# Optimization experiments

Measured on AMD Instinct MI355X. Metric: run time of the kernel, lower is better.

The kernel has to match this reference:

```python
import jax, jax.numpy as jnp
import numpy as np

B, S, M, E, H = 2, 2048, 2048, 1024, 16
D = E // H
LN_EPS = 1e-5


def setup_inputs() -> dict:
    key = jax.random.key(0)
    ks = jax.random.split(key, 14)
    w = lambda k: jax.random.normal(k, (E, E), dtype=jnp.float32) * 0.02
    return {
        "query": jax.random.normal(ks[0], (B, S, E), dtype=jnp.float32),
        "keys": jax.random.normal(ks[1], (B, M, E), dtype=jnp.float32),
        "values": jax.random.normal(ks[2], (B, M, E), dtype=jnp.float32),
        "Wq": w(ks[3]), "bq": jnp.zeros((E,), jnp.float32),
        "Wk": w(ks[4]), "bk": jnp.zeros((E,), jnp.float32),
        "Wv": w(ks[5]), "bv": jnp.zeros((E,), jnp.float32),
        "Wo": w(ks[6]), "bo": jnp.zeros((E,), jnp.float32),
        "gamma": jnp.ones((E,), jnp.float32),
        "beta": jnp.zeros((E,), jnp.float32),
    }


def reference(query, keys, values, Wq, bq, Wk, bk, Wv, bv, Wo, bo, gamma, beta):
    b, s, e = query.shape
    m = keys.shape[1]
    # projections (torch Linear: x @ W.T + b), split heads -> [b, H, len, D]
    Q = (jnp.einsum('bse,fe->bsf', query, Wq) + bq).reshape(b, s, H, D).transpose(0, 2, 1, 3)
    K = (jnp.einsum('bme,fe->bmf', keys, Wk) + bk).reshape(b, m, H, D).transpose(0, 2, 1, 3)
    V = (jnp.einsum('bme,fe->bmf', values, Wv) + bv).reshape(b, m, H, D).transpose(0, 2, 1, 3)
    scores = jnp.einsum('bhsd,bhmd->bhsm', Q, K) / np.sqrt(D).astype(np.float32)
    attn = jax.nn.softmax(scores, axis=-1)  # [b,H,s,m]; dropout is eval no-op
    attended = jnp.einsum('bhsm,bhmd->bhsd', attn, V)
    attended = attended.transpose(0, 2, 1, 3).reshape(b, s, e)
    y = jnp.einsum('bse,fe->bsf', attended, Wo) + bo + query
    mu = jnp.mean(y, axis=-1, keepdims=True)
    var = jnp.mean(jnp.square(y - mu), axis=-1, keepdims=True)
    out = (y - mu) * jax.lax.rsqrt(var + LN_EPS) * gamma + beta
    avg_attention = attn.mean(axis=1)  # [b,s,m]
    return out, avg_attention
```

## Files before the change

kernel.cpp:

```cpp
#include <hip/hip_runtime.h>
#include <hip/hip_bf16.h>

typedef unsigned short u16;
typedef unsigned int   u32;
typedef __attribute__((ext_vector_type(2)))  float fx2;
typedef __attribute__((ext_vector_type(4)))  float fx4;
typedef __attribute__((ext_vector_type(16))) float f32x16;
typedef __attribute__((ext_vector_type(4)))  u16   usx4;
typedef __attribute__((ext_vector_type(8)))  u16   usx8;
typedef __attribute__((ext_vector_type(8)))  __bf16 bf16x8;
typedef __attribute__((ext_vector_type(2)))  int   i32x2;
typedef __attribute__((ext_vector_type(2)))  u32   u32x2;
typedef __attribute__((ext_vector_type(4)))  u32   u32x4;

#define DEVI static __device__ __forceinline__

constexpr int Bb = 2, Ss = 2048, Mm = 2048, Ee = 1024, Hh = 16, Dd = 64;
#define QSCALE 0.18033688011112042f

DEVI u16 f2bf(float f) {
  u32 u = __builtin_bit_cast(u32, f);
  u32 r = (u + 0x7fffu + ((u >> 16) & 1u)) >> 16;
  return (u16)r;
}
DEVI bf16x8 as_bf(usx8 v) { return __builtin_bit_cast(bf16x8, v); }

DEVI void gld16(const u16* g, u16* l) {
  __builtin_amdgcn_global_load_lds((const __attribute__((address_space(1))) void*)g,
                                   (__attribute__((address_space(3))) void*)l, 16, 0, 0);
}

#if __has_builtin(__builtin_amdgcn_exp2f)
DEVI float xexp2(float x) { return __builtin_amdgcn_exp2f(x); }
#else
DEVI float xexp2(float x) { return exp2f(x); }
#endif

DEVI u32 cvtpk(float lo, float hi) {
  u32 r;
  asm("v_cvt_pk_bf16_f32 %0, %1, %2" : "=v"(r) : "v"(lo), "v"(hi));
  return r;
}
DEVI bf16x8 pa_from(u32 w0, u32 w1, u32 w2, u32 w3) {
  union { u32 u[4]; usx8 v; } t;
  t.u[0] = w0; t.u[1] = w1; t.u[2] = w2; t.u[3] = w3;
  return as_bf(t.v);
}

__global__ __launch_bounds__(256)
void cast_all(const float* __restrict__ q, const float* __restrict__ k,
              const float* __restrict__ v,
              const float* __restrict__ wq, const float* __restrict__ wk,
              const float* __restrict__ wv, const float* __restrict__ wo,
              u16* __restrict__ qc, u16* __restrict__ kc, u16* __restrict__ vc,
              u16* __restrict__ wqc, u16* __restrict__ wkc,
              u16* __restrict__ wvc, u16* __restrict__ woc)
{
  const int y = blockIdx.y;
  const float* s; u16* d; size_t n;
  const size_t NI = (size_t)Bb * Ss * Ee;
  const size_t NW = (size_t)Ee * Ee;
  switch (y) {
    case 0: s = q;  d = qc;  n = NI; break;
    case 1: s = k;  d = kc;  n = NI; break;
    case 2: s = v;  d = vc;  n = NI; break;
    case 3: s = wq; d = wqc; n = NW; break;
    case 4: s = wk; d = wkc; n = NW; break;
    case 5: s = wv; d = wvc; n = NW; break;
    default: s = wo; d = woc; n = NW; break;
  }
  const size_t stride = (size_t)gridDim.x * 256 * 8;
  for (size_t i = ((size_t)blockIdx.x * 256 + threadIdx.x) * 8; i < n; i += stride) {
    fx4 a = *(const fx4*)(s + i);
    fx4 b = *(const fx4*)(s + i + 4);
    u32x4 o;
    o[0] = cvtpk(a[0], a[1]); o[1] = cvtpk(a[2], a[3]);
    o[2] = cvtpk(b[0], b[1]); o[3] = cvtpk(b[2], b[3]);
    *(u32x4*)(d + i) = o;
  }
}

__global__ __launch_bounds__(256, 2)
void gemm_qkv(const u16* __restrict__ qc, const u16* __restrict__ kc,
              const u16* __restrict__ vc,
              const u16* __restrict__ wqc, const u16* __restrict__ wkc,
              const u16* __restrict__ wvc,
              const float* __restrict__ bq, const float* __restrict__ bk,
              const float* __restrict__ bv,
              u16* __restrict__ Qbf, u16* __restrict__ Kbf, u16* __restrict__ Vt)
{
  __shared__ u16 As[2][128][64];
  __shared__ u16 Bs[2][128][64];
  const int tid = threadIdx.x;
  const int w = tid >> 6, l = tid & 63, g = l >> 4, ln = l & 15;
  const int wr = w >> 1, wc = w & 1;

  const int lid = blockIdx.x;
  const int wg = (lid & 7) * 96 + (lid >> 3);
  const int z = wg >> 8;
  const int rem = wg & 255;
  const int row0 = (rem >> 3) * 128;
  const int col0 = (rem & 7) * 128;

  const u16* A = (z == 0) ? qc : (z == 1) ? kc : vc;
  const u16* W = (z == 0) ? wqc : (z == 1) ? wkc : wvc;
  const float* bias = (z == 0) ? bq : (z == 1) ? bk : bv;

  const int colu = (((l & 7) ^ (l >> 3)) << 3);
  auto stage = [&](int buf, int kt) {
#pragma unroll
    for (int j = 0; j < 4; j++) {
      const int c = j * 4 + w;
      const int row = c * 8 + (l >> 3);
      gld16(A + (size_t)(row0 + row) * 1024 + kt * 64 + colu,
            &As[buf][0][0] + c * 512 + l * 8);
      gld16(W + (size_t)(col0 + row) * 1024 + kt * 64 + colu,
            &Bs[buf][0][0] + c * 512 + l * 8);
    }
  };

  fx4 acc[4][4];
#pragma unroll
  for (int i = 0; i < 4; i++)
#pragma unroll
    for (int j = 0; j < 4; j++) acc[i][j] = fx4{0.f, 0.f, 0.f, 0.f};

  stage(0, 0);
  __syncthreads();

  const int swA = (ln & 7) << 3;
  const int NK = 1024 / 64;
  for (int kt = 0; kt < NK; kt++) {
    const int buf = kt & 1;
    if (kt + 1 < NK) stage(buf ^ 1, kt + 1);
#pragma unroll
    for (int ks = 0; ks < 2; ks++) {
      bf16x8 af[4], bfr[4];
      const int cb = (ks * 32 + g * 8) ^ swA;
#pragma unroll
      for (int mi = 0; mi < 4; mi++)
        af[mi] = as_bf(*(const usx8*)&As[buf][wr * 64 + mi * 16 + ln][cb]);
#pragma unroll
      for (int nj = 0; nj < 4; nj++)
        bfr[nj] = as_bf(*(const usx8*)&Bs[buf][wc * 64 + nj * 16 + ln][cb]);
      __builtin_amdgcn_s_setprio(1);
#pragma unroll
      for (int mi = 0; mi < 4; mi++)
#pragma unroll
        for (int nj = 0; nj < 4; nj++)
          acc[mi][nj] = __builtin_amdgcn_mfma_f32_16x16x32_bf16(af[mi], bfr[nj], acc[mi][nj], 0, 0, 0);
      __builtin_amdgcn_s_setprio(0);
    }
    __syncthreads();
  }

#pragma unroll
  for (int mi = 0; mi < 4; mi++) {
#pragma unroll
    for (int nj = 0; nj < 4; nj++) {
      const int j = col0 + wc * 64 + nj * 16 + ln;
      const float bj = bias[j];
      if (z == 2) {
        const int i0 = row0 + wr * 64 + mi * 16 + g * 4;
        const int b2 = i0 >> 11, m2 = i0 & 2047;
        const int h2 = j >> 6,  d2 = j & 63;
        u32x2 pk;
        pk[0] = cvtpk(acc[mi][nj][0] + bj, acc[mi][nj][1] + bj);
        pk[1] = cvtpk(acc[mi][nj][2] + bj, acc[mi][nj][3] + bj);
        *(u32x2*)&Vt[(((size_t)b2 * Hh + h2) * 64 + d2) * (size_t)Mm + m2] = pk;
      } else {
        u16* outp = (z == 0) ? Qbf : Kbf;
        const float sc = (z == 0) ? QSCALE : 1.0f;
#pragma unroll
        for (int r = 0; r < 4; r++) {
          const int i = row0 + wr * 64 + mi * 16 + g * 4 + r;
          outp[(size_t)i * 1024 + j] = f2bf((acc[mi][nj][r] + bj) * sc);
        }
      }
    }
  }
}

__global__ __launch_bounds__(256, 2)
void gemm_out(const u16* __restrict__ Ab, const u16* __restrict__ W,
              const float* __restrict__ bias, const float* __restrict__ resid,
              float* __restrict__ outf)
{
  __shared__ u16 As[2][128][64];
  __shared__ u16 Bs[2][128][64];
  const int tid = threadIdx.x;
  const int w = tid >> 6, l = tid & 63, g = l >> 4, ln = l & 15;
  const int wr = w >> 1, wc = w & 1;

  const int lid = blockIdx.x;
  const int wg = (lid & 7) * 32 + (lid >> 3);
  const int row0 = (wg >> 3) * 128;
  const int col0 = (wg & 7) * 128;

  const int colu = (((l & 7) ^ (l >> 3)) << 3);
  auto stage = [&](int buf, int kt) {
#pragma unroll
    for (int j = 0; j < 4; j++) {
      const int c = j * 4 + w;
      const int row = c * 8 + (l >> 3);
      gld16(Ab + (size_t)(row0 + row) * 1024 + kt * 64 + colu,
            &As[buf][0][0] + c * 512 + l * 8);
      gld16(W + (size_t)(col0 + row) * 1024 + kt * 64 + colu,
            &Bs[buf][0][0] + c * 512 + l * 8);
    }
  };

  fx4 acc[4][4];
#pragma unroll
  for (int i = 0; i < 4; i++)
#pragma unroll
    for (int j = 0; j < 4; j++) acc[i][j] = fx4{0.f, 0.f, 0.f, 0.f};

  stage(0, 0);
  __syncthreads();

  const int swA = (ln & 7) << 3;
  const int NK = 1024 / 64;
  for (int kt = 0; kt < NK; kt++) {
    const int buf = kt & 1;
    if (kt + 1 < NK) stage(buf ^ 1, kt + 1);
#pragma unroll
    for (int ks = 0; ks < 2; ks++) {
      bf16x8 af[4], bfr[4];
      const int cb = (ks * 32 + g * 8) ^ swA;
#pragma unroll
      for (int mi = 0; mi < 4; mi++)
        af[mi] = as_bf(*(const usx8*)&As[buf][wr * 64 + mi * 16 + ln][cb]);
#pragma unroll
      for (int nj = 0; nj < 4; nj++)
        bfr[nj] = as_bf(*(const usx8*)&Bs[buf][wc * 64 + nj * 16 + ln][cb]);
      __builtin_amdgcn_s_setprio(1);
#pragma unroll
      for (int mi = 0; mi < 4; mi++)
#pragma unroll
        for (int nj = 0; nj < 4; nj++)
          acc[mi][nj] = __builtin_amdgcn_mfma_f32_16x16x32_bf16(af[mi], bfr[nj], acc[mi][nj], 0, 0, 0);
      __builtin_amdgcn_s_setprio(0);
    }
    __syncthreads();
  }

#pragma unroll
  for (int mi = 0; mi < 4; mi++) {
#pragma unroll
    for (int nj = 0; nj < 4; nj++) {
      const int j = col0 + wc * 64 + nj * 16 + ln;
      const float bj = bias[j];
#pragma unroll
      for (int r = 0; r < 4; r++) {
        const int i = row0 + wr * 64 + mi * 16 + g * 4 + r;
        outf[(size_t)i * 1024 + j] = acc[mi][nj][r] + bj + resid[(size_t)i * 1024 + j];
      }
    }
  }
}

__global__ __launch_bounds__(256, 2)
void flash_fwd(const u16* __restrict__ Qb, const u16* __restrict__ Kb,
               const u16* __restrict__ Vt, u16* __restrict__ attended,
               float* __restrict__ stats)
{
  __shared__ u16 Ks[2][128][64];
  __shared__ u16 Vs[2][64][128];
  const int tid = threadIdx.x;
  const int w = tid >> 6, l = tid & 63;
  const int ln32 = l & 31, hi = l >> 5;
  const int st = blockIdx.x, h = blockIdx.y, b = blockIdx.z;
  const int s0 = st * 128 + w * 32;

  const u16* Kbase = Kb + (size_t)b * Mm * 1024 + h * 64;
  const u16* Vbase = Vt + ((size_t)(b * Hh + h) * 64) * (size_t)Mm;

  const int colu_k = (((l & 7) ^ (l >> 3)) << 3);
  auto stage = [&](int buf, int mt) {
    const int mb = mt * 128;
#pragma unroll
    for (int j = 0; j < 4; j++) {
      const int c = j * 4 + w;
      const int krow = c * 8 + (l >> 3);
      gld16(Kbase + (size_t)(mb + krow) * 1024 + colu_k,
            &Ks[buf][0][0] + c * 512 + l * 8);
      const int vrow = c * 4 + (l >> 4);
      const int colv = (((l & 15) ^ (vrow & 15)) << 3);
      gld16(Vbase + (size_t)vrow * (size_t)Mm + mb + colv,
            &Vs[buf][0][0] + c * 512 + l * 8);
    }
  };

  bf16x8 qa[4];
#pragma unroll
  for (int dstep = 0; dstep < 4; dstep++)
    qa[dstep] = as_bf(*(const usx8*)(Qb + (size_t)(b * Ss + s0 + ln32) * Ee
                                     + h * 64 + dstep * 16 + hi * 8));

  f32x16 acc[2];
#pragma unroll
  for (int i = 0; i < 16; i++) { acc[0][i] = 0.f; acc[1][i] = 0.f; }
  float lsum = 0.f;

  stage(0, 0);
  __syncthreads();

  const int NT = Mm / 128;
  for (int mt = 0; mt < NT; mt++) {
    const int buf = mt & 1;
    if (mt + 1 < NT) stage(buf ^ 1, mt + 1);

    f32x16 sc[4];
#pragma unroll
    for (int mtile = 0; mtile < 4; mtile++) {
      const int row = mtile * 32 + ln32;
      const int sw = (row & 7) << 3;
      f32x16 c;
#pragma unroll
      for (int i = 0; i < 16; i++) c[i] = 0.f;
#pragma unroll
      for (int dstep = 0; dstep < 4; dstep++) {
        bf16x8 kf = as_bf(*(const usx8*)&Ks[buf][row][(dstep * 16 + hi * 8) ^ sw]);
        c = __builtin_amdgcn_mfma_f32_32x32x16_bf16(kf, qa[dstep], c, 0, 0, 0);
      }
      sc[mtile] = c;
    }

#pragma unroll
    for (int mtile = 0; mtile < 4; mtile++) {
      float p[16];
#pragma unroll
      for (int r = 0; r < 16; r++) p[r] = xexp2(sc[mtile][r]);
      float t0 = (p[0] + p[1]) + (p[2] + p[3]);
      float t1 = (p[4] + p[5]) + (p[6] + p[7]);
      float t2 = (p[8] + p[9]) + (p[10] + p[11]);
      float t3 = (p[12] + p[13]) + (p[14] + p[15]);
      lsum += (t0 + t1) + (t2 + t3);

      u32 cp[8];
#pragma unroll
      for (int i = 0; i < 8; i++) cp[i] = cvtpk(p[2 * i], p[2 * i + 1]);
      i32x2 sA = __builtin_amdgcn_permlane32_swap((int)cp[0], (int)cp[2], false, false);
      i32x2 sB = __builtin_amdgcn_permlane32_swap((int)cp[1], (int)cp[3], false, false);
      bf16x8 pa0 = pa_from((u32)sA.x, (u32)sB.x, (u32)sA.y, (u32)sB.y);
      i32x2 sC = __builtin_amdgcn_permlane32_swap((int)cp[4], (int)cp[6], false, false);
      i32x2 sD = __builtin_amdgcn_permlane32_swap((int)cp[5], (int)cp[7], false, false);
      bf16x8 pa1 = pa_from((u32)sC.x, (u32)sD.x, (u32)sC.y, (u32)sD.y);

#pragma unroll
      for (int dtile = 0; dtile < 2; dtile++) {
        const int vrow = dtile * 32 + ln32;
        const int vsw = (vrow & 15) << 3;
        bf16x8 vb0 = as_bf(*(const usx8*)&Vs[buf][vrow][(mtile * 32 + hi * 8) ^ vsw]);
        bf16x8 vb1 = as_bf(*(const usx8*)&Vs[buf][vrow][(mtile * 32 + 16 + hi * 8) ^ vsw]);
        acc[dtile] = __builtin_amdgcn_mfma_f32_32x32x16_bf16(pa0, vb0, acc[dtile], 0, 0, 0);
        acc[dtile] = __builtin_amdgcn_mfma_f32_32x32x16_bf16(pa1, vb1, acc[dtile], 0, 0, 0);
      }
    }
    __syncthreads();
  }

  lsum += __shfl_xor(lsum, 32);
  const float inv = 1.0f / lsum;
  if (l < 32)
    stats[(size_t)(b * Hh + h) * Ss + s0 + l] = inv;
#pragma unroll
  for (int r = 0; r < 16; r++) {
    const int srow = (r & 3) + 8 * (r >> 2) + 4 * hi;
    const float invr = __shfl(inv, srow);
    const int s_abs = s0 + srow;
#pragma unroll
    for (int dtile = 0; dtile < 2; dtile++)
      attended[(size_t)(b * Ss + s_abs) * Ee + h * 64 + dtile * 32 + ln32] =
          f2bf(acc[dtile][r] * invr);
  }
}

__global__ __launch_bounds__(256)
void avg_attn(const u16* __restrict__ Qb, const u16* __restrict__ Kb,
              const float* __restrict__ stats, float* __restrict__ avg_out)
{
  __shared__ u16 Ks[2][64][64];
  const int tid = threadIdx.x;
  const int w = tid >> 6, l = tid & 63;
  const int ln32 = l & 31, hi = l >> 5;
  const int mtile0 = blockIdx.x, stile = blockIdx.y, b = blockIdx.z;
  const int m0 = mtile0 * 64;
  const int s0 = stile * 128 + w * 32;
  const int s_lane = s0 + ln32;

  const u16* Kbase = Kb + (size_t)(b * Mm + m0) * 1024;
  const u16* Qrow  = Qb + (size_t)(b * Ss + s_lane) * Ee;
  const float* strow = stats + (size_t)b * Hh * Ss + s_lane;

  const int colu = (((l & 7) ^ (l >> 3)) << 3);
  auto stage = [&](int buf, int h) {
#pragma unroll
    for (int j = 0; j < 2; j++) {
      const int c = j * 4 + w;
      const int row = c * 8 + (l >> 3);
      u16* kdst = &Ks[buf][0][0] + c * 512 + l * 8;
      gld16(Kbase + (size_t)row * 1024 + h * 64 + colu, kdst);
    }
  };

  f32x16 acc[2];
#pragma unroll
  for (int i = 0; i < 16; i++) { acc[0][i] = 0.f; acc[1][i] = 0.f; }

  stage(0, 0);
  __syncthreads();

  for (int h = 0; h < Hh; h++) {
    const int buf = h & 1;
    if (h + 1 < Hh) stage(buf ^ 1, h + 1);

    bf16x8 qa[4];
#pragma unroll
    for (int dstep = 0; dstep < 4; dstep++)
      qa[dstep] = as_bf(*(const usx8*)(Qrow + h * 64 + dstep * 16 + hi * 8));
    const float invh = strow[(size_t)h * Ss];

#pragma unroll
    for (int mtile = 0; mtile < 2; mtile++) {
      const int row = mtile * 32 + ln32;
      const int sw = (row & 7) << 3;
      f32x16 c;
#pragma unroll
      for (int i = 0; i < 16; i++) c[i] = 0.f;
      __builtin_amdgcn_s_setprio(1);
#pragma unroll
      for (int dstep = 0; dstep < 4; dstep++) {
        bf16x8 kf = as_bf(*(const usx8*)&Ks[buf][row][(dstep * 16 + hi * 8) ^ sw]);
        c = __builtin_amdgcn_mfma_f32_32x32x16_bf16(kf, qa[dstep], c, 0, 0, 0);
      }
      __builtin_amdgcn_s_setprio(0);
#pragma unroll
      for (int r = 0; r < 16; r++)
        acc[mtile][r] += xexp2(c[r]) * invh;
    }
    __syncthreads();
  }

  float* orow = avg_out + ((size_t)(b * Ss + s_lane)) * Mm + m0;
#pragma unroll
  for (int mtile = 0; mtile < 2; mtile++)
#pragma unroll
    for (int rq = 0; rq < 4; rq++) {
      fx4 o;
#pragma unroll
      for (int j = 0; j < 4; j++) o[j] = acc[mtile][rq * 4 + j] * (1.0f / 16.0f);
      *(fx4*)(orow + mtile * 32 + rq * 8 + 4 * hi) = o;
    }
}

__global__ __launch_bounds__(256)
void ln_kernel(const float* __restrict__ y, const float* __restrict__ gamma,
               const float* __restrict__ beta, float* __restrict__ out)
{
  const int row = blockIdx.x, tid = threadIdx.x;
  const int w = tid >> 6, l = tid & 63;
  fx4 v = *(const fx4*)(y + (size_t)row * 1024 + tid * 4);
  float s = v[0] + v[1] + v[2] + v[3];
  float s2 = v[0] * v[0] + v[1] * v[1] + v[2] * v[2] + v[3] * v[3];
#pragma unroll
  for (int off = 32; off >= 1; off >>= 1) {
    s += __shfl_xor(s, off);
    s2 += __shfl_xor(s2, off);
  }
  __shared__ float rs[4], rq[4];
  if (l == 0) { rs[w] = s; rq[w] = s2; }
  __syncthreads();
  s = (rs[0] + rs[1]) + (rs[2] + rs[3]);
  s2 = (rq[0] + rq[1]) + (rq[2] + rq[3]);
  const float mu = s * (1.0f / 1024.0f);
  const float var = s2 * (1.0f / 1024.0f) - mu * mu;
  const float rstd = rsqrtf(var + 1e-5f);
  fx4 gm = *(const fx4*)(gamma + tid * 4);
  fx4 bt = *(const fx4*)(beta + tid * 4);
  fx4 o;
#pragma unroll
  for (int j = 0; j < 4; j++) o[j] = (v[j] - mu) * rstd * gm[j] + bt[j];
  *(fx4*)(out + (size_t)row * 1024 + tid * 4) = o;
}

extern "C" void kernel_launch(void* const* d_in, const int* in_sizes, int n_in,
                              void* d_out, int out_size, void* d_ws, size_t ws_size,
                              hipStream_t stream)
{
  const float* query = (const float*)d_in[0];
  const float* keys  = (const float*)d_in[1];
  const float* values = (const float*)d_in[2];
  const float* Wq = (const float*)d_in[3];  const float* bq = (const float*)d_in[4];
  const float* Wk = (const float*)d_in[5];  const float* bk = (const float*)d_in[6];
  const float* Wv = (const float*)d_in[7];  const float* bv = (const float*)d_in[8];
  const float* Wo = (const float*)d_in[9];  const float* bo = (const float*)d_in[10];
  const float* gamma = (const float*)d_in[11];
  const float* beta  = (const float*)d_in[12];

  float* out = (float*)d_out;
  float* avg_out = out + (size_t)Bb * Ss * Ee;

  const size_t MB = 1024 * 1024;
  char* ws = (char*)d_ws;
  u16*   Qbf    = (u16*)(ws);
  u16*   Kbf    = (u16*)(ws + 8  * MB);
  u16*   Vt     = (u16*)(ws + 16 * MB);
  u16*   qc     = (u16*)(ws + 24 * MB);
  u16*   kc     = (u16*)(ws + 32 * MB);
  u16*   vc     = (u16*)(ws + 40 * MB);
  u16*   wqc    = (u16*)(ws + 48 * MB);
  u16*   wkc    = (u16*)(ws + 50 * MB);
  u16*   wvc    = (u16*)(ws + 52 * MB);
  u16*   woc    = (u16*)(ws + 54 * MB);
  float* stats  = (float*)(ws + 56 * MB);
  u16*   att_bf = (u16*)(ws + 24 * MB);
  float* ybuf   = (float*)(ws);

  cast_all<<<dim3(512, 7), 256, 0, stream>>>(query, keys, values, Wq, Wk, Wv, Wo,
                                             qc, kc, vc, wqc, wkc, wvc, woc);

  gemm_qkv<<<dim3(768), 256, 0, stream>>>(qc, kc, vc, wqc, wkc, wvc,
                                          bq, bk, bv, Qbf, Kbf, Vt);

  flash_fwd<<<dim3(Ss / 128, Hh, Bb), 256, 0, stream>>>(Qbf, Kbf, Vt, att_bf, stats);
  avg_attn<<<dim3(Mm / 64, Ss / 128, Bb), 256, 0, stream>>>(Qbf, Kbf, stats, avg_out);

  gemm_out<<<dim3(256), 256, 0, stream>>>(att_bf, woc, bo, query, ybuf);
  ln_kernel<<<dim3(Bb * Ss), 256, 0, stream>>>(ybuf, gamma, beta, out);
}
```

Before: 173.5 us.

## Shrink avg_attn M tile, swizzle block order for XCD locality, prefetch Q and stats

The avg_attn kernel now covers 32 key rows per block instead of 64, which doubles the grid to 2048 blocks on a flat 1D launch. The linear block id is remapped so that neighbouring blocks on the same XCD (lid&7 interleave) share the same K tile and differ only in S tile, aiming for better L2 reuse of K. Q fragments for the next head are prefetched into registers, and all 16 per-head normaliser stats are loaded once up front. This is meant to raise occupancy and hide load latency. In exchange, each Q row is reloaded twice as many times across the grid, and the larger grid adds per-block overhead.

```diff
diff --git a/kernel.cpp b/kernel.cpp
--- a/kernel.cpp
+++ b/kernel.cpp
@@ -381,78 +381,85 @@
 void avg_attn(const u16* __restrict__ Qb, const u16* __restrict__ Kb,
               const float* __restrict__ stats, float* __restrict__ avg_out)
 {
-  __shared__ u16 Ks[2][64][64];
+  __shared__ u16 Ks[2][32][64];
   const int tid = threadIdx.x;
   const int w = tid >> 6, l = tid & 63;
   const int ln32 = l & 31, hi = l >> 5;
-  const int mtile0 = blockIdx.x, stile = blockIdx.y, b = blockIdx.z;
-  const int m0 = mtile0 * 64;
-  const int s0 = stile * 128 + w * 32;
+
+  const int lid = blockIdx.x;
+  const int wg = (lid & 7) * 256 + (lid >> 3);
+  const int st = wg & 15;
+  const int mt = (wg >> 4) & 63;
+  const int b  = wg >> 10;
+  const int m0 = mt * 32;
+  const int s0 = st * 128 + w * 32;
   const int s_lane = s0 + ln32;
 
   const u16* Kbase = Kb + (size_t)(b * Mm + m0) * 1024;
   const u16* Qrow  = Qb + (size_t)(b * Ss + s_lane) * Ee;
   const float* strow = stats + (size_t)b * Hh * Ss + s_lane;
 
-  const int colu = (((l & 7) ^ (l >> 3)) << 3);
+  float invs[16];
+#pragma unroll
+  for (int h = 0; h < Hh; h++) invs[h] = strow[(size_t)h * Ss];
+
+  const int srow_st = tid >> 3;
+  const int colu = (((tid & 7) ^ (srow_st & 7)) << 3);
   auto stage = [&](int buf, int h) {
-#pragma unroll
-    for (int j = 0; j < 2; j++) {
-      const int c = j * 4 + w;
-      const int row = c * 8 + (l >> 3);
-      u16* kdst = &Ks[buf][0][0] + c * 512 + l * 8;
-      gld16(Kbase + (size_t)row * 1024 + h * 64 + colu, kdst);
-    }
+    gld16(Kbase + (size_t)srow_st * 1024 + h * 64 + colu,
+          &Ks[buf][0][0] + tid * 8);
   };
 
-  f32x16 acc[2];
-#pragma unroll
-  for (int i = 0; i < 16; i++) { acc[0][i] = 0.f; acc[1][i] = 0.f; }
-
+  auto loadQ = [&](bf16x8* qa, int h) {
+#pragma unroll
+    for (int d = 0; d < 4; d++)
+      qa[d] = as_bf(*(const usx8*)(Qrow + h * 64 + d * 16 + hi * 8));
+  };
+
+  f32x16 acc;
+#pragma unroll
+  for (int i = 0; i < 16; i++) acc[i] = 0.f;
+
+  bf16x8 qnow[4], qnxt[4];
+  loadQ(qnow, 0);
   stage(0, 0);
   __syncthreads();
 
+  const int row = ln32;
+  const int sw = (row & 7) << 3;
+#pragma unroll
   for (int h = 0; h < Hh; h++) {
     const int buf = h & 1;
-    if (h + 1 < Hh) stage(buf ^ 1, h + 1);
-
-    bf16x8 qa[4];
-#pragma unroll
-    for (int dstep = 0; dstep < 4; dstep++)
-      qa[dstep] = as_bf(*(const usx8*)(Qrow + h * 64 + dstep * 16 + hi * 8));
-    const float invh = strow[(size_t)h * Ss];
-
-#pragma unroll
-    for (int mtile = 0; mtile < 2; mtile++) {
-      const int row = mtile * 32 + ln32;
-      const int sw = (row & 7) << 3;
-      f32x16 c;
-#pragma unroll
-      for (int i = 0; i < 16; i++) c[i] = 0.f;
-      __builtin_amdgcn_s_setprio(1);
-#pragma unroll
-      for (int dstep = 0; dstep < 4; dstep++) {
-        bf16x8 kf = as_bf(*(const usx8*)&Ks[buf][row][(dstep * 16 + hi * 8) ^ sw]);
-        c = __builtin_amdgcn_mfma_f32_32x32x16_bf16(kf, qa[dstep], c, 0, 0, 0);
-      }
-      __builtin_amdgcn_s_setprio(0);
-#pragma unroll
-      for (int r = 0; r < 16; r++)
-        acc[mtile][r] += xexp2(c[r]) * invh;
-    }
+    if (h + 1 < Hh) { stage(buf ^ 1, h + 1); loadQ(qnxt, h + 1); }
+
+    f32x16 c;
+#pragma unroll
+    for (int i = 0; i < 16; i++) c[i] = 0.f;
+    __builtin_amdgcn_s_setprio(1);
+#pragma unroll
+    for (int dstep = 0; dstep < 4; dstep++) {
+      bf16x8 kf = as_bf(*(const usx8*)&Ks[buf][row][(dstep * 16 + hi * 8) ^ sw]);
+      c = __builtin_amdgcn_mfma_f32_32x32x16_bf16(kf, qnow[dstep], c, 0, 0, 0);
+    }
+    __builtin_amdgcn_s_setprio(0);
+    const float invh = invs[h];
+#pragma unroll
+    for (int r = 0; r < 16; r++)
+      acc[r] += xexp2(c[r]) * invh;
+
     __syncthreads();
+#pragma unroll
+    for (int d = 0; d < 4; d++) qnow[d] = qnxt[d];
   }
 
   float* orow = avg_out + ((size_t)(b * Ss + s_lane)) * Mm + m0;
 #pragma unroll
-  for (int mtile = 0; mtile < 2; mtile++)
-#pragma unroll
-    for (int rq = 0; rq < 4; rq++) {
-      fx4 o;
-#pragma unroll
-      for (int j = 0; j < 4; j++) o[j] = acc[mtile][rq * 4 + j] * (1.0f / 16.0f);
-      *(fx4*)(orow + mtile * 32 + rq * 8 + 4 * hi) = o;
-    }
+  for (int rq = 0; rq < 4; rq++) {
+    fx4 o;
+#pragma unroll
+    for (int j = 0; j < 4; j++) o[j] = acc[rq * 4 + j] * (1.0f / 16.0f);
+    *(fx4*)(orow + rq * 8 + 4 * hi) = o;
+  }
 }
 
 __global__ __launch_bounds__(256)
@@ -525,7 +532,7 @@
                                           bq, bk, bv, Qbf, Kbf, Vt);
 
   flash_fwd<<<dim3(Ss / 128, Hh, Bb), 256, 0, stream>>>(Qbf, Kbf, Vt, att_bf, stats);
-  avg_attn<<<dim3(Mm / 64, Ss / 128, Bb), 256, 0, stream>>>(Qbf, Kbf, stats, avg_out);
+  avg_attn<<<dim3(2048), 256, 0, stream>>>(Qbf, Kbf, stats, avg_out);
 
   gemm_out<<<dim3(256), 256, 0, stream>>>(att_bf, woc, bo, query, ybuf);
   ln_kernel<<<dim3(Bb * Ss), 256, 0, stream>>>(ybuf, gamma, beta, out);
```

Result: slower. 243.7 us (+40.5%).
